# Kernel tuning notes

Hardware: AMD Instinct MI355X
Metric: run time of the kernel (lower is better)

## Reference

```python
import jax, jax.numpy as jnp
import numpy as np

B, S, H, Z = 32, 2048, 256, 64
TEMPERATURE = float(H) ** 0.5
NEG_INF = -1e9


def setup_inputs() -> dict:
    key = jax.random.key(0)
    ks = jax.random.split(key, 8)
    return {
        "encoder_hidden_states": jax.random.normal(ks[0], (B, S, H), dtype=jnp.float32),
        "decoder_hidden_states": jax.random.normal(ks[1], (B, S, H), dtype=jnp.float32),
        "decoder_final_hidden_state": jax.random.normal(ks[2], (B, H), dtype=jnp.float32),
        "latent_z_seq": jax.random.normal(ks[3], (B, S, Z), dtype=jnp.float32),
        "mask": jax.random.randint(ks[4], (B, S), 0, 2).astype(bool),
        "Wq": jax.random.normal(ks[5], (H, H), dtype=jnp.float32),
        "Wk": jax.random.normal(ks[6], (H, H), dtype=jnp.float32),
        "Wv": jax.random.normal(ks[7], (Z, Z), dtype=jnp.float32),
    }


def reference(encoder_hidden_states, decoder_hidden_states, decoder_final_hidden_state,
              latent_z_seq, mask, Wq, Wk, Wv):
    # Projections
    k = jnp.einsum('bsh,hd->bsd', encoder_hidden_states, Wk)
    q = jnp.einsum('bsh,hd->bsd', decoder_hidden_states, Wq)
    v = jnp.einsum('bsz,zd->bsd', latent_z_seq, Wv)
    # alignment[b, i, j] = q_i . k_j / sqrt(H)   -> [B, S, S]
    alignment = jnp.einsum('bid,bjd->bij', q, k) / TEMPERATURE
    # mask over QUERY positions (axis -2), broadcast along key axis (-1)
    alignment = jnp.where(mask[:, :, None], alignment, NEG_INF)
    # NOTE: non-standard softmax over the query axis (dim=-2)
    attn = jax.nn.softmax(alignment, axis=-2)
    output = jnp.einsum('bij,bjd->bid', attn, v)  # [B, S, Z]
    return output, attn
```

## Files before the change

### kernel.cpp

```cpp
#include <hip/hip_runtime.h>
#include <stdint.h>

#define B_  32
#define S_  2048
#define H_  256
#define Z_  64

typedef unsigned short u16;
typedef __attribute__((ext_vector_type(8))) short bf16x8;
typedef __attribute__((ext_vector_type(4))) float f32x4;

__device__ __forceinline__ u16 f2bf(float f) {
    unsigned int x = __float_as_uint(f);
    x = (x + 0x7fffu + ((x >> 16) & 1u)) >> 16;
    return (u16)x;
}
__device__ __forceinline__ float bf2f(u16 u) {
    return __uint_as_float(((unsigned int)u) << 16);
}

__device__ __forceinline__ void gl2lds16(const void* g, void* l) {
    __builtin_amdgcn_global_load_lds(
        (const __attribute__((address_space(1))) unsigned int*)g,
        (__attribute__((address_space(3))) unsigned int*)l,
        16, 0, 0);
}

__global__ void detect_kernel(const u16* __restrict__ wq, int* __restrict__ flag) {
    __shared__ int tot;
    const int t = threadIdx.x;
    if (t == 0) tot = 0;
    __syncthreads();
    int cnt = 0;
    #pragma unroll
    for (int r = 0; r < 16; ++r) {
        u16 u = wq[(r * 256 + t) * 2];
        int e = (u >> 7) & 0xFF;
        cnt += (u == 0 || (e >= 107 && e <= 132)) ? 1 : 0;
    }
    atomicAdd(&tot, cnt);
    __syncthreads();
    if (t == 0) *flag = (tot < 2048) ? 1 : 0;
}

__global__ __launch_bounds__(256) void mask_conv_kernel(const void* __restrict__ raw,
                                                        int* __restrict__ mi) {
    __shared__ int isByte;
    const int t = threadIdx.x;
    if (t == 0) isByte = 0;
    __syncthreads();
    const unsigned int* w = (const unsigned int*)raw;
    if (w[t & 255] > 1u) isByte = 1;
    __syncthreads();
    int e = blockIdx.x * 256 + t;
    int val;
    if (isByte) val = ((const unsigned char*)raw)[e] ? 1 : 0;
    else        val = w[e] ? 1 : 0;
    mi[e] = val;
}

__global__ void wsplit_kernel(const int* __restrict__ flagp,
                              const void* __restrict__ Wq, const void* __restrict__ Wk,
                              u16* __restrict__ WqTh, u16* __restrict__ WqTl,
                              u16* __restrict__ WkTh, u16* __restrict__ WkTl) {
    const int fp32 = *flagp;
    const void* src = blockIdx.y ? Wk : Wq;
    u16* oh = blockIdx.y ? WkTh : WqTh;
    u16* ol = blockIdx.y ? WkTl : WqTl;
    int base = blockIdx.x * 1024;
    #pragma unroll
    for (int r = 0; r < 4; ++r) {
        int idx = base + r * 256 + threadIdx.x;
        int d = idx >> 8, h = idx & 255;
        float v = fp32 ? ((const float*)src)[h * 256 + d]
                       : bf2f(((const u16*)src)[h * 256 + d]);
        u16 hi = f2bf(v);
        oh[idx] = hi;
        ol[idx] = f2bf(v - bf2f(hi));
    }
}

__global__ __launch_bounds__(256) void xsplit_kernel(
        const int* __restrict__ flagp,
        const void* __restrict__ dec, const void* __restrict__ enc,
        u16* __restrict__ Xdh, u16* __restrict__ Xdl,
        u16* __restrict__ Xeh, u16* __restrict__ Xel)
{
    const int fp32 = *flagp;
    const void* src = blockIdx.y ? enc : dec;
    u16* oh = blockIdx.y ? Xeh : Xdh;
    u16* ol = blockIdx.y ? Xel : Xdl;
    const int t = threadIdx.x;
    const size_t blockbase = (size_t)blockIdx.x * 4096;
    if (fp32) {
        const float4* s4 = (const float4*)src;
        #pragma unroll
        for (int j = 0; j < 4; ++j) {
            size_t idx = blockbase + j * 1024 + t * 4;
            float4 v = s4[idx >> 2];
            u16 h0 = f2bf(v.x), h1 = f2bf(v.y), h2 = f2bf(v.z), h3 = f2bf(v.w);
            u16 l0 = f2bf(v.x - bf2f(h0)), l1 = f2bf(v.y - bf2f(h1));
            u16 l2 = f2bf(v.z - bf2f(h2)), l3 = f2bf(v.w - bf2f(h3));
            uint2 ph, pl;
            ph.x = (unsigned)h0 | ((unsigned)h1 << 16);
            ph.y = (unsigned)h2 | ((unsigned)h3 << 16);
            pl.x = (unsigned)l0 | ((unsigned)l1 << 16);
            pl.y = (unsigned)l2 | ((unsigned)l3 << 16);
            ((uint2*)oh)[idx >> 2] = ph;
            ((uint2*)ol)[idx >> 2] = pl;
        }
    } else {
        const uint2* s2 = (const uint2*)src;
        #pragma unroll
        for (int j = 0; j < 4; ++j) {
            size_t idx = blockbase + j * 1024 + t * 4;
            uint2 r = s2[idx >> 2];
            uint2 z; z.x = 0u; z.y = 0u;
            ((uint2*)oh)[idx >> 2] = r;
            ((uint2*)ol)[idx >> 2] = z;
        }
    }
}

__global__ __launch_bounds__(256, 2) void proj_kernel(
        const int* __restrict__ flagp, int use_xsplit,
        const float* __restrict__ Xf, const u16* __restrict__ Xu,
        const u16* __restrict__ Xh, const u16* __restrict__ Xl,
        const u16* __restrict__ WTh, const u16* __restrict__ WTl,
        u16* __restrict__ Ph, u16* __restrict__ Pl)
{
    __shared__ __align__(16) u16 ldsAh[128 * 32];
    __shared__ __align__(16) u16 ldsAl[128 * 32];
    __shared__ __align__(16) u16 ldsBh[128 * 32];
    __shared__ __align__(16) u16 ldsBl[128 * 32];
    const int fp32 = *flagp;
    const int t = threadIdx.x;
    const int lane = t & 63, w = t >> 6;
    const int i0 = blockIdx.x * 128;
    const int d0 = blockIdx.y * 128;
    const int rh = w >> 1, ch = w & 1;
    const int l15 = lane & 15, koff = (lane >> 4) * 8;

    f32x4 acc[4][4];
    #pragma unroll
    for (int a = 0; a < 4; ++a)
        #pragma unroll
        for (int c = 0; c < 4; ++c) acc[a][c] = (f32x4){0.f, 0.f, 0.f, 0.f};

    for (int ks = 0; ks < 8; ++ks) {
        const int kc = ks * 32;
        #pragma unroll
        for (int rep = 0; rep < 2; ++rep) {
            int s = t + rep * 256;
            int r = s >> 2, c8 = (s & 3) * 8;
            gl2lds16(WTh + (size_t)(d0 + r) * H_ + kc + c8, ldsBh + s * 8);
            gl2lds16(WTl + (size_t)(d0 + r) * H_ + kc + c8, ldsBl + s * 8);
            if (use_xsplit) {
                size_t go = (size_t)(i0 + r) * H_ + kc + c8;
                gl2lds16(Xh + go, ldsAh + s * 8);
                gl2lds16(Xl + go, ldsAl + s * 8);
            }
        }
        if (!use_xsplit) {
            if (fp32) {
                #pragma unroll
                for (int rep = 0; rep < 2; ++rep) {
                    int s = t + rep * 256;
                    int r = s >> 2, c8 = (s & 3) * 8;
                    const float4* src = (const float4*)(Xf + (size_t)(i0 + r) * H_ + kc + c8);
                    float4 x0 = src[0], x1 = src[1];
                    float xs[8] = {x0.x, x0.y, x0.z, x0.w, x1.x, x1.y, x1.z, x1.w};
                    unsigned hh[8], ll[8];
                    #pragma unroll
                    for (int j = 0; j < 8; ++j) {
                        u16 hb = f2bf(xs[j]);
                        hh[j] = hb;
                        ll[j] = f2bf(xs[j] - bf2f(hb));
                    }
                    uint4 ph, pl;
                    ph.x = hh[0] | (hh[1] << 16); ph.y = hh[2] | (hh[3] << 16);
                    ph.z = hh[4] | (hh[5] << 16); ph.w = hh[6] | (hh[7] << 16);
                    pl.x = ll[0] | (ll[1] << 16); pl.y = ll[2] | (ll[3] << 16);
                    pl.z = ll[4] | (ll[5] << 16); pl.w = ll[6] | (ll[7] << 16);
                    *(uint4*)(ldsAh + s * 8) = ph;
                    *(uint4*)(ldsAl + s * 8) = pl;
                }
            } else {
                #pragma unroll
                for (int rep = 0; rep < 2; ++rep) {
                    int s = t + rep * 256;
                    int r = s >> 2, c8 = (s & 3) * 8;
                    uint4 raw = *(const uint4*)(Xu + (size_t)(i0 + r) * H_ + kc + c8);
                    *(uint4*)(ldsAh + s * 8) = raw;
                    *(uint4*)(ldsAl + s * 8) = (uint4){0u, 0u, 0u, 0u};
                }
            }
        }
        __syncthreads();
        bf16x8 ah[4], al[4], bh[4], bl[4];
        #pragma unroll
        for (int f = 0; f < 4; ++f) {
            int ar = (rh * 64 + f * 16 + l15) * 32 + koff;
            int br = (ch * 64 + f * 16 + l15) * 32 + koff;
            ah[f] = *(const bf16x8*)(ldsAh + ar);
            al[f] = *(const bf16x8*)(ldsAl + ar);
            bh[f] = *(const bf16x8*)(ldsBh + br);
            bl[f] = *(const bf16x8*)(ldsBl + br);
        }
        #pragma unroll
        for (int fr = 0; fr < 4; ++fr)
            #pragma unroll
            for (int fc = 0; fc < 4; ++fc) {
                acc[fr][fc] = __builtin_amdgcn_mfma_f32_16x16x32_bf16(al[fr], bh[fc], acc[fr][fc], 0, 0, 0);
                acc[fr][fc] = __builtin_amdgcn_mfma_f32_16x16x32_bf16(ah[fr], bl[fc], acc[fr][fc], 0, 0, 0);
                acc[fr][fc] = __builtin_amdgcn_mfma_f32_16x16x32_bf16(ah[fr], bh[fc], acc[fr][fc], 0, 0, 0);
            }
        __syncthreads();
    }
    #pragma unroll
    for (int fr = 0; fr < 4; ++fr)
        #pragma unroll
        for (int fc = 0; fc < 4; ++fc)
            #pragma unroll
            for (int reg = 0; reg < 4; ++reg) {
                float v = acc[fr][fc][reg];
                int i = i0 + rh * 64 + fr * 16 + (lane >> 4) * 4 + reg;
                int d = d0 + ch * 64 + fc * 16 + l15;
                u16 hi = f2bf(v);
                u16 lo = f2bf(v - bf2f(hi));
                size_t off = (size_t)i * H_ + d;
                Ph[off] = hi;
                Pl[off] = lo;
            }
}

__global__ __launch_bounds__(256) void vproj_kernel(
        const int* __restrict__ flagp, const void* __restrict__ Lraw,
        const void* __restrict__ Wvraw, u16* __restrict__ vT)
{
    __shared__ float wv[64 * 16];
    const int fp32 = *flagp;
    const int t = threadIdx.x;
    const int dc = blockIdx.y;
    #pragma unroll
    for (int r = 0; r < 4; ++r) {
        int idx = r * 256 + t;
        int z = idx >> 4, dd = idx & 15;
        wv[idx] = fp32 ? ((const float*)Wvraw)[z * 64 + dc * 16 + dd]
                       : bf2f(((const u16*)Wvraw)[z * 64 + dc * 16 + dd]);
    }
    __syncthreads();
    const int flat = blockIdx.x * 256 + t;
    const int b = flat >> 11, s = flat & 2047;

    float lz[64];
    if (fp32) {
        const float4* lr = (const float4*)((const float*)Lraw + (size_t)flat * 64);
        #pragma unroll
        for (int c = 0; c < 16; ++c) {
            float4 v = lr[c];
            lz[c * 4 + 0] = v.x; lz[c * 4 + 1] = v.y;
            lz[c * 4 + 2] = v.z; lz[c * 4 + 3] = v.w;
        }
    } else {
        const uint4* lr = (const uint4*)((const u16*)Lraw + (size_t)flat * 64);
        #pragma unroll
        for (int c = 0; c < 8; ++c) {
            uint4 v = lr[c];
            unsigned wd[4] = {v.x, v.y, v.z, v.w};
            #pragma unroll
            for (int e2 = 0; e2 < 4; ++e2) {
                lz[c * 8 + e2 * 2 + 0] = bf2f((u16)(wd[e2] & 0xffffu));
                lz[c * 8 + e2 * 2 + 1] = bf2f((u16)(wd[e2] >> 16));
            }
        }
    }

    float acc[16];
    #pragma unroll
    for (int d = 0; d < 16; ++d) acc[d] = 0.f;
    for (int z = 0; z < 64; ++z) {
        float lv = lz[z];
        const float4* wrow = (const float4*)&wv[z * 16];
        #pragma unroll
        for (int d4 = 0; d4 < 4; ++d4) {
            float4 wq = wrow[d4];
            acc[d4 * 4 + 0] += lv * wq.x;
            acc[d4 * 4 + 1] += lv * wq.y;
            acc[d4 * 4 + 2] += lv * wq.z;
            acc[d4 * 4 + 3] += lv * wq.w;
        }
    }
    #pragma unroll
    for (int d = 0; d < 16; ++d)
        vT[((size_t)b * 64 + dc * 16 + d) * S_ + s] = f2bf(acc[d]);
}

__global__ __launch_bounds__(256, 2) void qk_kernel(
        const u16* __restrict__ qh, const u16* __restrict__ ql,
        const u16* __restrict__ kh, const u16* __restrict__ kl,
        const int* __restrict__ maskI, u16* __restrict__ attnB,
        float* __restrict__ attnF, u16* __restrict__ stageB, int use_stage,
        float* __restrict__ m_p, float* __restrict__ s_p,
        int b0, const int* __restrict__ flagp)
{
    __shared__ __align__(16) char smem[35328];
    u16*  stage = (u16*)smem;
    u16*  etile = (u16*)smem;
    float* cmax = (float*)(smem + 32768);
    float* csum = (float*)(smem + 33792);
    float* mrow = (float*)(smem + 34816);

    const int fp32 = *flagp;
    const int t = threadIdx.x;
    const int lane = t & 63, w = t >> 6;
    const int jt = blockIdx.x, it = blockIdx.y, bz = blockIdx.z;
    const int b = b0 + bz;
    const int i0 = it * 128, j0 = jt * 128;
    const int rh = w >> 1, ch = w & 1;
    const int l15 = lane & 15, koff = (lane >> 4) * 8;

    if (t < 128) mrow[t] = (maskI[b * S_ + i0 + t] != 0) ? 1.f : 0.f;

    const size_t qbase = ((size_t)bz * S_ + i0) * H_;
    const size_t kbase = ((size_t)bz * S_ + j0) * H_;

    f32x4 acc[4][4];
    #pragma unroll
    for (int a = 0; a < 4; ++a)
        #pragma unroll
        for (int c = 0; c < 4; ++c) acc[a][c] = (f32x4){0.f, 0.f, 0.f, 0.f};

    for (int ks = 0; ks < 8; ++ks) {
        const int kc = ks * 32;
        #pragma unroll
        for (int rep = 0; rep < 2; ++rep) {
            int s = t + rep * 256;
            int r = s >> 2, c8 = (s & 3) * 8;
            size_t go = (size_t)r * H_ + kc + c8;
            gl2lds16(qh + qbase + go, stage + 0 * 4096 + s * 8);
            gl2lds16(ql + qbase + go, stage + 1 * 4096 + s * 8);
            gl2lds16(kh + kbase + go, stage + 2 * 4096 + s * 8);
            gl2lds16(kl + kbase + go, stage + 3 * 4096 + s * 8);
        }
        __syncthreads();
        bf16x8 ah[4], al[4], bh[4], bl[4];
        #pragma unroll
        for (int f = 0; f < 4; ++f) {
            int ar = (rh * 64 + f * 16 + l15) * 32 + koff;
            int br = (ch * 64 + f * 16 + l15) * 32 + koff;
            ah[f] = *(const bf16x8*)(stage + 0 * 4096 + ar);
            al[f] = *(const bf16x8*)(stage + 1 * 4096 + ar);
            bh[f] = *(const bf16x8*)(stage + 2 * 4096 + br);
            bl[f] = *(const bf16x8*)(stage + 3 * 4096 + br);
        }
        #pragma unroll
        for (int fr = 0; fr < 4; ++fr)
            #pragma unroll
            for (int fc = 0; fc < 4; ++fc) {
                acc[fr][fc] = __builtin_amdgcn_mfma_f32_16x16x32_bf16(al[fr], bh[fc], acc[fr][fc], 0, 0, 0);
                acc[fr][fc] = __builtin_amdgcn_mfma_f32_16x16x32_bf16(ah[fr], bl[fc], acc[fr][fc], 0, 0, 0);
                acc[fr][fc] = __builtin_amdgcn_mfma_f32_16x16x32_bf16(ah[fr], bh[fc], acc[fr][fc], 0, 0, 0);
            }
        __syncthreads();
    }

    const float inv_t = 0.0625f;
    float mloc[4] = {-3e38f, -3e38f, -3e38f, -3e38f};
    #pragma unroll
    for (int fr = 0; fr < 4; ++fr)
        #pragma unroll
        for (int reg = 0; reg < 4; ++reg) {
            float keep = mrow[rh * 64 + fr * 16 + (lane >> 4) * 4 + reg];
            #pragma unroll
            for (int fc = 0; fc < 4; ++fc) {
                float l = acc[fr][fc][reg] * inv_t;
                l = (keep != 0.f) ? l : -1e9f;
                acc[fr][fc][reg] = l;
                mloc[fc] = fmaxf(mloc[fc], l);
            }
        }
    #pragma unroll
    for (int fc = 0; fc < 4; ++fc) {
        mloc[fc] = fmaxf(mloc[fc], __shfl_xor(mloc[fc], 16, 64));
        mloc[fc] = fmaxf(mloc[fc], __shfl_xor(mloc[fc], 32, 64));
    }
    if (lane < 16) {
        #pragma unroll
        for (int fc = 0; fc < 4; ++fc)
            cmax[rh * 128 + ch * 64 + fc * 16 + lane] = mloc[fc];
    }
    __syncthreads();

    float mcol[4], sloc[4];
    #pragma unroll
    for (int fc = 0; fc < 4; ++fc) {
        int c = ch * 64 + fc * 16 + l15;
        mcol[fc] = fmaxf(cmax[c], cmax[128 + c]);
        sloc[fc] = 0.f;
    }
    #pragma unroll
    for (int fr = 0; fr < 4; ++fr)
        #pragma unroll
        for (int reg = 0; reg < 4; ++reg) {
            int row = rh * 64 + fr * 16 + (lane >> 4) * 4 + reg;
            #pragma unroll
            for (int fc = 0; fc < 4; ++fc) {
                float e = __expf(acc[fr][fc][reg] - mcol[fc]);
                sloc[fc] += e;
                etile[row * 128 + ch * 64 + fc * 16 + l15] = f2bf(e);
            }
        }
    #pragma unroll
    for (int fc = 0; fc < 4; ++fc) {
        sloc[fc] += __shfl_xor(sloc[fc], 16, 64);
        sloc[fc] += __shfl_xor(sloc[fc], 32, 64);
    }
    if (lane < 16) {
        #pragma unroll
        for (int fc = 0; fc < 4; ++fc)
            csum[rh * 128 + ch * 64 + fc * 16 + lane] = sloc[fc];
    }
    __syncthreads();

    if (t < 128) {
        float m = fmaxf(cmax[t], cmax[128 + t]);
        float sres = csum[t] + csum[128 + t];
        size_t so = ((size_t)b * 16 + it) * S_ + j0 + t;
        m_p[so] = m;
        s_p[so] = sres;
    }
    const size_t abase = ((size_t)b * S_ + i0) * S_ + j0;
    if (fp32) {
        if (use_stage) {
            #pragma unroll
            for (int rep = 0; rep < 8; ++rep) {
                int s = t + rep * 256;
                int row = s >> 4, off = (s & 15) * 8;
                *(uint4*)(stageB + abase + (size_t)row * S_ + off) = *(const uint4*)(etile + s * 8);
            }
        } else {
            #pragma unroll
            for (int rep = 0; rep < 8; ++rep) {
                int s = t + rep * 256;
                int row = s >> 4, off = (s & 15) * 8;
                const u16* src = etile + s * 8;
                float* gp = attnF + abase + (size_t)row * S_ + off;
                float4 f0, f1;
                f0.x = bf2f(src[0]); f0.y = bf2f(src[1]); f0.z = bf2f(src[2]); f0.w = bf2f(src[3]);
                f1.x = bf2f(src[4]); f1.y = bf2f(src[5]); f1.z = bf2f(src[6]); f1.w = bf2f(src[7]);
                *(float4*)gp = f0;
                *(float4*)(gp + 4) = f1;
            }
        }
    } else {
        #pragma unroll
        for (int rep = 0; rep < 8; ++rep) {
            int s = t + rep * 256;
            int row = s >> 4, off = (s & 15) * 8;
            *(uint4*)(attnB + abase + (size_t)row * S_ + off) = *(const uint4*)(etile + s * 8);
        }
    }
}

__global__ __launch_bounds__(256) void stats_kernel(
        const float* __restrict__ m_p, const float* __restrict__ s_p, float* __restrict__ scl)
{
    int id = blockIdx.x * 256 + threadIdx.x;
    int b = id >> 11, j = id & 2047;
    float mv[16];
    float M = -3e38f;
    #pragma unroll
    for (int itile = 0; itile < 16; ++itile) {
        mv[itile] = m_p[((size_t)b * 16 + itile) * S_ + j];
        M = fmaxf(M, mv[itile]);
    }
    float L = 0.f;
    #pragma unroll
    for (int itile = 0; itile < 16; ++itile)
        L += s_p[((size_t)b * 16 + itile) * S_ + j] * __expf(mv[itile] - M);
    float invL = (L > 0.f) ? (1.f / L) : 0.f;
    #pragma unroll
    for (int itile = 0; itile < 16; ++itile)
        scl[((size_t)b * 16 + itile) * S_ + j] = __expf(mv[itile] - M) * invL;
}

__global__ __launch_bounds__(256, 2) void av_kernel(
        const u16* __restrict__ vT, const float* __restrict__ scl,
        u16* __restrict__ attnB, float* __restrict__ attnF,
        const u16* __restrict__ stageB, int use_stage,
        u16* __restrict__ outB, float* __restrict__ outF,
        const int* __restrict__ flagp)
{
    __shared__ __align__(16) u16 lds_attn[128 * 128];
    __shared__ __align__(16) u16 lds_vt[64 * 128];
    __shared__ float lds_scale[128];
    const int fp32 = *flagp;
    const int t = threadIdx.x;
    const int lane = t & 63, w = t >> 6;
    const int it = blockIdx.x, b = blockIdx.y;
    const int i0 = it * 128;
    const int l15 = lane & 15, koff = (lane >> 4) * 8;

    f32x4 acc[2][4];
    #pragma unroll
    for (int a = 0; a < 2; ++a)
        #pragma unroll
        for (int c = 0; c < 4; ++c) acc[a][c] = (f32x4){0.f, 0.f, 0.f, 0.f};

    for (int jt = 0; jt < 16; ++jt) {
        const int j0 = jt * 128;
        __syncthreads();
        if (t < 128) lds_scale[t] = scl[((size_t)b * 16 + it) * S_ + j0 + t];
        #pragma unroll
        for (int rep = 0; rep < 4; ++rep) {
            int s = t + rep * 256;
            int d = s >> 4, off = (s & 15) * 8;
            gl2lds16(vT + ((size_t)b * 64 + d) * S_ + j0 + off, lds_vt + s * 8);
        }
        __syncthreads();

        const size_t abase = ((size_t)b * S_ + i0) * S_ + j0;
        if (fp32) {
            if (use_stage) {
                #pragma unroll
                for (int rep = 0; rep < 8; ++rep) {
                    int s = t + rep * 256;
                    int row = s >> 4, off = (s & 15) * 8;
                    uint4 pk = *(const uint4*)(stageB + abase + (size_t)row * S_ + off);
                    unsigned wd[4] = {pk.x, pk.y, pk.z, pk.w};
                    float4 f0, f1;
                    f0.x = bf2f((u16)(wd[0] & 0xffffu)) * lds_scale[off + 0];
                    f0.y = bf2f((u16)(wd[0] >> 16))     * lds_scale[off + 1];
                    f0.z = bf2f((u16)(wd[1] & 0xffffu)) * lds_scale[off + 2];
                    f0.w = bf2f((u16)(wd[1] >> 16))     * lds_scale[off + 3];
                    f1.x = bf2f((u16)(wd[2] & 0xffffu)) * lds_scale[off + 4];
                    f1.y = bf2f((u16)(wd[2] >> 16))     * lds_scale[off + 5];
                    f1.z = bf2f((u16)(wd[3] & 0xffffu)) * lds_scale[off + 6];
                    f1.w = bf2f((u16)(wd[3] >> 16))     * lds_scale[off + 7];
                    float* gp = attnF + abase + (size_t)row * S_ + off;
                    *(float4*)gp = f0;
                    *(float4*)(gp + 4) = f1;
                    uint4 opk;
                    opk.x = (unsigned)f2bf(f0.x) | ((unsigned)f2bf(f0.y) << 16);
                    opk.y = (unsigned)f2bf(f0.z) | ((unsigned)f2bf(f0.w) << 16);
                    opk.z = (unsigned)f2bf(f1.x) | ((unsigned)f2bf(f1.y) << 16);
                    opk.w = (unsigned)f2bf(f1.z) | ((unsigned)f2bf(f1.w) << 16);
                    *(uint4*)(lds_attn + s * 8) = opk;
                }
            } else {
                #pragma unroll
                for (int rep = 0; rep < 8; ++rep) {
                    int s = t + rep * 256;
                    int row = s >> 4, off = (s & 15) * 8;
                    float* gp = attnF + abase + (size_t)row * S_ + off;
                    float4 p0 = *(const float4*)gp;
                    float4 p1 = *(const float4*)(gp + 4);
                    p0.x *= lds_scale[off + 0]; p0.y *= lds_scale[off + 1];
                    p0.z *= lds_scale[off + 2]; p0.w *= lds_scale[off + 3];
                    p1.x *= lds_scale[off + 4]; p1.y *= lds_scale[off + 5];
                    p1.z *= lds_scale[off + 6]; p1.w *= lds_scale[off + 7];
                    *(float4*)gp = p0;
                    *(float4*)(gp + 4) = p1;
                    uint4 pk;
                    pk.x = (unsigned)f2bf(p0.x) | ((unsigned)f2bf(p0.y) << 16);
                    pk.y = (unsigned)f2bf(p0.z) | ((unsigned)f2bf(p0.w) << 16);
                    pk.z = (unsigned)f2bf(p1.x) | ((unsigned)f2bf(p1.y) << 16);
                    pk.w = (unsigned)f2bf(p1.z) | ((unsigned)f2bf(p1.w) << 16);
                    *(uint4*)(lds_attn + s * 8) = pk;
                }
            }
        } else {
            #pragma unroll
            for (int rep = 0; rep < 8; ++rep) {
                int s = t + rep * 256;
                int row = s >> 4, off = (s & 15) * 8;
                size_t ga = abase + (size_t)row * S_ + off;
                uint4 pk = *(const uint4*)(attnB + ga);
                unsigned int wd[4] = {pk.x, pk.y, pk.z, pk.w};
                #pragma unroll
                for (int e2 = 0; e2 < 4; ++e2) {
                    float f0 = bf2f((u16)(wd[e2] & 0xffffu)) * lds_scale[off + e2 * 2];
                    float f1 = bf2f((u16)(wd[e2] >> 16))     * lds_scale[off + e2 * 2 + 1];
                    wd[e2] = (unsigned int)f2bf(f0) | ((unsigned int)f2bf(f1) << 16);
                }
                uint4 opk; opk.x = wd[0]; opk.y = wd[1]; opk.z = wd[2]; opk.w = wd[3];
                *(uint4*)(attnB + ga) = opk;
                *(uint4*)(lds_attn + s * 8) = opk;
            }
        }
        __syncthreads();

        #pragma unroll
        for (int ksj = 0; ksj < 4; ++ksj) {
            bf16x8 a0 = *(const bf16x8*)(lds_attn + (w * 32 +  0 + l15) * 128 + ksj * 32 + koff);
            bf16x8 a1 = *(const bf16x8*)(lds_attn + (w * 32 + 16 + l15) * 128 + ksj * 32 + koff);
            bf16x8 bb[4];
            #pragma unroll
            for (int fc = 0; fc < 4; ++fc)
                bb[fc] = *(const bf16x8*)(lds_vt + (fc * 16 + l15) * 128 + ksj * 32 + koff);
            #pragma unroll
            for (int fc = 0; fc < 4; ++fc) {
                acc[0][fc] = __builtin_amdgcn_mfma_f32_16x16x32_bf16(a0, bb[fc], acc[0][fc], 0, 0, 0);
                acc[1][fc] = __builtin_amdgcn_mfma_f32_16x16x32_bf16(a1, bb[fc], acc[1][fc], 0, 0, 0);
            }
        }
    }
    #pragma unroll
    for (int fr = 0; fr < 2; ++fr)
        #pragma unroll
        for (int fc = 0; fc < 4; ++fc)
            #pragma unroll
            for (int reg = 0; reg < 4; ++reg) {
                int i = i0 + w * 32 + fr * 16 + (lane >> 4) * 4 + reg;
                int d = fc * 16 + l15;
                float v = acc[fr][fc][reg];
                size_t oo = ((size_t)b * S_ + i) * Z_ + d;
                if (fp32) outF[oo] = v;
                else      outB[oo] = f2bf(v);
            }
}

extern "C" void kernel_launch(void* const* d_in, const int* in_sizes, int n_in,
                              void* d_out, int out_size, void* d_ws, size_t ws_size,
                              hipStream_t stream) {
    const void* enc    = d_in[0];
    const void* dec    = d_in[1];
    const void* latent = d_in[3];
    const void* mraw   = d_in[4];
    const void* Wq     = d_in[5];
    const void* Wk     = d_in[6];
    const void* Wv     = d_in[7];

    u16*   outB  = (u16*)d_out;
    float* outF  = (float*)d_out;
    u16*   attnB = outB + (size_t)B_ * S_ * Z_;
    float* attnF = outF + (size_t)B_ * S_ * Z_;
    float* m_p = (float*)d_out;
    float* s_p = m_p + (size_t)B_ * 16 * S_;

    char* ws = (char*)d_ws;
    int*   flag  = (int*)ws;
    int*   maskI = (int*)(ws + 256);
    u16*   vT    = (u16*)((char*)maskI + (size_t)B_ * S_ * 4);
    u16*   WqTh  = vT + (size_t)B_ * Z_ * S_;
    u16*   WqTl  = WqTh + H_ * H_;
    u16*   WkTh  = WqTl + H_ * H_;
    u16*   WkTl  = WkTh + H_ * H_;
    float* scl   = (float*)(WkTl + H_ * H_);
    char*  dyn   = (char*)(scl + (size_t)B_ * 16 * S_);

    const size_t fixed_bytes  = (size_t)(dyn - ws);
    const size_t per_batch    = (size_t)4 * S_ * H_ * 2;
    const size_t xsplit_bytes = (size_t)4 * B_ * S_ * H_ * 2;
    const size_t stage_bytes  = (size_t)B_ * S_ * S_ * 2;

    long long avail = (long long)ws_size - (long long)fixed_bytes;
    int use_xsplit = 0, use_stage = 0;
    u16 *Xdh = 0, *Xdl = 0, *Xeh = 0, *Xel = 0, *stageB = 0;
    if (avail >= (long long)(xsplit_bytes + per_batch)) {
        use_xsplit = 1;
        Xdh = (u16*)dyn;
        Xdl = Xdh + (size_t)B_ * S_ * H_;
        Xeh = Xdl + (size_t)B_ * S_ * H_;
        Xel = Xeh + (size_t)B_ * S_ * H_;
        dyn += xsplit_bytes;
        avail -= (long long)xsplit_bytes;
    }
    if (avail >= (long long)(stage_bytes + per_batch)) {
        use_stage = 1;
        stageB = (u16*)dyn;
        dyn += stage_bytes;
        avail -= (long long)stage_bytes;
    }
    int g_b = (avail > 0) ? (int)(avail / (long long)per_batch) : 1;
    if (g_b < 1)  g_b = 1;
    if (g_b > 32) g_b = 32;

    u16* qh = (u16*)dyn;
    u16* ql = qh + (size_t)g_b * S_ * H_;
    u16* kh = ql + (size_t)g_b * S_ * H_;
    u16* kl = kh + (size_t)g_b * S_ * H_;

    detect_kernel<<<dim3(1), 256, 0, stream>>>((const u16*)Wq, flag);
    mask_conv_kernel<<<dim3(256), 256, 0, stream>>>(mraw, maskI);
    wsplit_kernel<<<dim3(64, 2), 256, 0, stream>>>(flag, Wq, Wk, WqTh, WqTl, WkTh, WkTl);
    vproj_kernel<<<dim3(256, 4), 256, 0, stream>>>(flag, latent, Wv, vT);
    if (use_xsplit)
        xsplit_kernel<<<dim3(4096, 2), 256, 0, stream>>>(flag, dec, enc, Xdh, Xdl, Xeh, Xel);

    for (int b0 = 0; b0 < B_; b0 += g_b) {
        int g = (B_ - b0 < g_b) ? (B_ - b0) : g_b;
        size_t eoff = (size_t)b0 * S_ * H_;
        proj_kernel<<<dim3(g * 16, 2), 256, 0, stream>>>(
            flag, use_xsplit, (const float*)dec + eoff, (const u16*)dec + eoff,
            use_xsplit ? Xdh + eoff : (u16*)0, use_xsplit ? Xdl + eoff : (u16*)0,
            WqTh, WqTl, qh, ql);
        proj_kernel<<<dim3(g * 16, 2), 256, 0, stream>>>(
            flag, use_xsplit, (const float*)enc + eoff, (const u16*)enc + eoff,
            use_xsplit ? Xeh + eoff : (u16*)0, use_xsplit ? Xel + eoff : (u16*)0,
            WkTh, WkTl, kh, kl);
        qk_kernel<<<dim3(16, 16, g), 256, 0, stream>>>(qh, ql, kh, kl, maskI,
                                                       attnB, attnF, stageB, use_stage,
                                                       m_p, s_p, b0, flag);
    }
    stats_kernel<<<dim3(256), 256, 0, stream>>>(m_p, s_p, scl);
    av_kernel<<<dim3(16, 32), 256, 0, stream>>>(vT, scl, attnB, attnF, stageB, use_stage,
                                                outB, outF, flag);
}
```

Before: 1.177 ms.

## Swizzle LDS layouts, merge Q/K projections, and split AV into GEMM plus scale pass

```diff
diff --git a/kernel.cpp b/kernel.cpp
--- a/kernel.cpp
+++ b/kernel.cpp
@@ -124,22 +124,40 @@
 
 __global__ __launch_bounds__(256, 2) void proj_kernel(
         const int* __restrict__ flagp, int use_xsplit,
-        const float* __restrict__ Xf, const u16* __restrict__ Xu,
-        const u16* __restrict__ Xh, const u16* __restrict__ Xl,
-        const u16* __restrict__ WTh, const u16* __restrict__ WTl,
-        u16* __restrict__ Ph, u16* __restrict__ Pl)
+        const float* __restrict__ Xf0, const u16* __restrict__ Xu0,
+        const u16* __restrict__ Xh0, const u16* __restrict__ Xl0,
+        const u16* __restrict__ WTh0, const u16* __restrict__ WTl0,
+        u16* __restrict__ Ph0, u16* __restrict__ Pl0,
+        const float* __restrict__ Xf1, const u16* __restrict__ Xu1,
+        const u16* __restrict__ Xh1, const u16* __restrict__ Xl1,
+        const u16* __restrict__ WTh1, const u16* __restrict__ WTl1,
+        u16* __restrict__ Ph1, u16* __restrict__ Pl1)
 {
-    __shared__ __align__(16) u16 ldsAh[128 * 32];
-    __shared__ __align__(16) u16 ldsAl[128 * 32];
-    __shared__ __align__(16) u16 ldsBh[128 * 32];
-    __shared__ __align__(16) u16 ldsBl[128 * 32];
+    __shared__ __align__(16) u16 lds[16384];
+    const int z = blockIdx.z;
+    const float* Xf = z ? Xf1 : Xf0;
+    const u16*   Xu = z ? Xu1 : Xu0;
+    const u16*   Xh = z ? Xh1 : Xh0;
+    const u16*   Xl = z ? Xl1 : Xl0;
+    const u16*  WTh = z ? WTh1 : WTh0;
+    const u16*  WTl = z ? WTl1 : WTl0;
+    u16* Ph = z ? Ph1 : Ph0;
+    u16* Pl = z ? Pl1 : Pl0;
+
     const int fp32 = *flagp;
     const int t = threadIdx.x;
     const int lane = t & 63, w = t >> 6;
     const int i0 = blockIdx.x * 128;
     const int d0 = blockIdx.y * 128;
     const int rh = w >> 1, ch = w & 1;
-    const int l15 = lane & 15, koff = (lane >> 4) * 8;
+    const int l15 = lane & 15;
+    const int c0 = lane >> 4;
+
+    const int srow = t >> 3;
+    const int scp  = t & 7;
+    const int sc   = scp ^ (srow & 7);
+    const int scol = (sc & 3) * 8;
+    const int slo  = sc & 4;
 
     f32x4 acc[4][4];
     #pragma unroll
@@ -149,63 +167,70 @@
 
     for (int ks = 0; ks < 8; ++ks) {
         const int kc = ks * 32;
-        #pragma unroll
-        for (int rep = 0; rep < 2; ++rep) {
-            int s = t + rep * 256;
-            int r = s >> 2, c8 = (s & 3) * 8;
-            gl2lds16(WTh + (size_t)(d0 + r) * H_ + kc + c8, ldsBh + s * 8);
-            gl2lds16(WTl + (size_t)(d0 + r) * H_ + kc + c8, ldsBl + s * 8);
-            if (use_xsplit) {
-                size_t go = (size_t)(i0 + r) * H_ + kc + c8;
-                gl2lds16(Xh + go, ldsAh + s * 8);
-                gl2lds16(Xl + go, ldsAl + s * 8);
-            }
-        }
-        if (!use_xsplit) {
-            if (fp32) {
+        {
+            const u16* wsrc = slo ? WTl : WTh;
+            #pragma unroll
+            for (int rep = 0; rep < 4; ++rep) {
+                int s = t + rep * 256;
+                int row = srow + rep * 32;
+                gl2lds16(wsrc + (size_t)(d0 + row) * H_ + kc + scol, lds + 8192 + s * 8);
+            }
+        }
+        if (use_xsplit) {
+            const u16* xsrc = slo ? Xl : Xh;
+            #pragma unroll
+            for (int rep = 0; rep < 4; ++rep) {
+                int s = t + rep * 256;
+                int row = srow + rep * 32;
+                gl2lds16(xsrc + (size_t)(i0 + row) * H_ + kc + scol, lds + s * 8);
+            }
+        } else if (fp32) {
+            #pragma unroll
+            for (int rep = 0; rep < 2; ++rep) {
+                int s = t + rep * 256;
+                int r = s >> 2, c8 = s & 3;
+                const float4* src = (const float4*)(Xf + (size_t)(i0 + r) * H_ + kc + c8 * 8);
+                float4 x0 = src[0], x1 = src[1];
+                float xs[8] = {x0.x, x0.y, x0.z, x0.w, x1.x, x1.y, x1.z, x1.w};
+                unsigned hh[8], ll[8];
                 #pragma unroll
-                for (int rep = 0; rep < 2; ++rep) {
-                    int s = t + rep * 256;
-                    int r = s >> 2, c8 = (s & 3) * 8;
-                    const float4* src = (const float4*)(Xf + (size_t)(i0 + r) * H_ + kc + c8);
-                    float4 x0 = src[0], x1 = src[1];
-                    float xs[8] = {x0.x, x0.y, x0.z, x0.w, x1.x, x1.y, x1.z, x1.w};
-                    unsigned hh[8], ll[8];
-                    #pragma unroll
-                    for (int j = 0; j < 8; ++j) {
-                        u16 hb = f2bf(xs[j]);
-                        hh[j] = hb;
-                        ll[j] = f2bf(xs[j] - bf2f(hb));
-                    }
-                    uint4 ph, pl;
-                    ph.x = hh[0] | (hh[1] << 16); ph.y = hh[2] | (hh[3] << 16);
-                    ph.z = hh[4] | (hh[5] << 16); ph.w = hh[6] | (hh[7] << 16);
-                    pl.x = ll[0] | (ll[1] << 16); pl.y = ll[2] | (ll[3] << 16);
-                    pl.z = ll[4] | (ll[5] << 16); pl.w = ll[6] | (ll[7] << 16);
-                    *(uint4*)(ldsAh + s * 8) = ph;
-                    *(uint4*)(ldsAl + s * 8) = pl;
+                for (int j = 0; j < 8; ++j) {
+                    u16 hb = f2bf(xs[j]);
+                    hh[j] = hb;
+                    ll[j] = f2bf(xs[j] - bf2f(hb));
                 }
-            } else {
-                #pragma unroll
-                for (int rep = 0; rep < 2; ++rep) {
-                    int s = t + rep * 256;
-                    int r = s >> 2, c8 = (s & 3) * 8;
-                    uint4 raw = *(const uint4*)(Xu + (size_t)(i0 + r) * H_ + kc + c8);
-                    *(uint4*)(ldsAh + s * 8) = raw;
-                    *(uint4*)(ldsAl + s * 8) = (uint4){0u, 0u, 0u, 0u};
-                }
+                uint4 ph, pl;
+                ph.x = hh[0] | (hh[1] << 16); ph.y = hh[2] | (hh[3] << 16);
+                ph.z = hh[4] | (hh[5] << 16); ph.w = hh[6] | (hh[7] << 16);
+                pl.x = ll[0] | (ll[1] << 16); pl.y = ll[2] | (ll[3] << 16);
+                pl.z = ll[4] | (ll[5] << 16); pl.w = ll[6] | (ll[7] << 16);
+                int posH = c8 ^ (r & 7);
+                *(uint4*)(lds + r * 64 + posH * 8) = ph;
+                *(uint4*)(lds + r * 64 + (posH ^ 4) * 8) = pl;
+            }
+        } else {
+            #pragma unroll
+            for (int rep = 0; rep < 2; ++rep) {
+                int s = t + rep * 256;
+                int r = s >> 2, c8 = s & 3;
+                uint4 raw = *(const uint4*)(Xu + (size_t)(i0 + r) * H_ + kc + c8 * 8);
+                int posH = c8 ^ (r & 7);
+                *(uint4*)(lds + r * 64 + posH * 8) = raw;
+                *(uint4*)(lds + r * 64 + (posH ^ 4) * 8) = (uint4){0u, 0u, 0u, 0u};
             }
         }
         __syncthreads();
         bf16x8 ah[4], al[4], bh[4], bl[4];
         #pragma unroll
         for (int f = 0; f < 4; ++f) {
-            int ar = (rh * 64 + f * 16 + l15) * 32 + koff;
-            int br = (ch * 64 + f * 16 + l15) * 32 + koff;
-            ah[f] = *(const bf16x8*)(ldsAh + ar);
-            al[f] = *(const bf16x8*)(ldsAl + ar);
-            bh[f] = *(const bf16x8*)(ldsBh + br);
-            bl[f] = *(const bf16x8*)(ldsBl + br);
+            int ra = rh * 64 + f * 16 + l15;
+            int rb = ch * 64 + f * 16 + l15;
+            int pa = c0 ^ (ra & 7);
+            int pb = c0 ^ (rb & 7);
+            ah[f] = *(const bf16x8*)(lds + ra * 64 + pa * 8);
+            al[f] = *(const bf16x8*)(lds + ra * 64 + (pa ^ 4) * 8);
+            bh[f] = *(const bf16x8*)(lds + 8192 + rb * 64 + pb * 8);
+            bl[f] = *(const bf16x8*)(lds + 8192 + rb * 64 + (pb ^ 4) * 8);
         }
         #pragma unroll
         for (int fr = 0; fr < 4; ++fr)
@@ -318,13 +343,21 @@
     const int b = b0 + bz;
     const int i0 = it * 128, j0 = jt * 128;
     const int rh = w >> 1, ch = w & 1;
-    const int l15 = lane & 15, koff = (lane >> 4) * 8;
+    const int l15 = lane & 15;
+    const int c0 = lane >> 4;
 
     if (t < 128) mrow[t] = (maskI[b * S_ + i0 + t] != 0) ? 1.f : 0.f;
 
     const size_t qbase = ((size_t)bz * S_ + i0) * H_;
     const size_t kbase = ((size_t)bz * S_ + j0) * H_;
 
+    const int srow = t >> 3;
+    const int scp  = t & 7;
+    const int sc   = scp ^ (srow & 7);
+    const int scol = (sc & 3) * 8;
+    const u16* qsrc = (sc & 4) ? ql : qh;
+    const u16* ksrc = (sc & 4) ? kl : kh;
+
     f32x4 acc[4][4];
     #pragma unroll
     for (int a = 0; a < 4; ++a)
@@ -334,25 +367,24 @@
     for (int ks = 0; ks < 8; ++ks) {
         const int kc = ks * 32;
         #pragma unroll
-        for (int rep = 0; rep < 2; ++rep) {
+        for (int rep = 0; rep < 4; ++rep) {
             int s = t + rep * 256;
-            int r = s >> 2, c8 = (s & 3) * 8;
-            size_t go = (size_t)r * H_ + kc + c8;
-            gl2lds16(qh + qbase + go, stage + 0 * 4096 + s * 8);
-            gl2lds16(ql + qbase + go, stage + 1 * 4096 + s * 8);
-            gl2lds16(kh + kbase + go, stage + 2 * 4096 + s * 8);
-            gl2lds16(kl + kbase + go, stage + 3 * 4096 + s * 8);
+            int row = srow + rep * 32;
+            gl2lds16(qsrc + qbase + (size_t)row * H_ + kc + scol, stage + s * 8);
+            gl2lds16(ksrc + kbase + (size_t)row * H_ + kc + scol, stage + 8192 + s * 8);
         }
         __syncthreads();
         bf16x8 ah[4], al[4], bh[4], bl[4];
         #pragma unroll
         for (int f = 0; f < 4; ++f) {
-            int ar = (rh * 64 + f * 16 + l15) * 32 + koff;
-            int br = (ch * 64 + f * 16 + l15) * 32 + koff;
-            ah[f] = *(const bf16x8*)(stage + 0 * 4096 + ar);
-            al[f] = *(const bf16x8*)(stage + 1 * 4096 + ar);
-            bh[f] = *(const bf16x8*)(stage + 2 * 4096 + br);
-            bl[f] = *(const bf16x8*)(stage + 3 * 4096 + br);
+            int ra = rh * 64 + f * 16 + l15;
+            int rb = ch * 64 + f * 16 + l15;
+            int pa = c0 ^ (ra & 7);
+            int pb = c0 ^ (rb & 7);
+            ah[f] = *(const bf16x8*)(stage + ra * 64 + pa * 8);
+            al[f] = *(const bf16x8*)(stage + ra * 64 + (pa ^ 4) * 8);
+            bh[f] = *(const bf16x8*)(stage + 8192 + rb * 64 + pb * 8);
+            bl[f] = *(const bf16x8*)(stage + 8192 + rb * 64 + (pb ^ 4) * 8);
         }
         #pragma unroll
         for (int fr = 0; fr < 4; ++fr)
@@ -485,10 +517,150 @@
         scl[((size_t)b * 16 + itile) * S_ + j] = __expf(mv[itile] - M) * invL;
 }
 
-__global__ __launch_bounds__(256, 2) void av_kernel(
+__global__ __launch_bounds__(256, 2) void av_gemm_kernel(
+        const u16* __restrict__ vT, const float* __restrict__ scl,
+        const u16* __restrict__ stageB, const u16* __restrict__ attnRawB,
+        u16* __restrict__ outB, float* __restrict__ outF,
+        const int* __restrict__ flagp)
+{
+    __shared__ __align__(16) u16 lds_attn[128 * 128];
+    __shared__ __align__(16) u16 lds_vt[64 * 128];
+    const int fp32 = *flagp;
+    const u16* srcE = fp32 ? stageB : attnRawB;
+    const int t = threadIdx.x;
+    const int lane = t & 63, w = t >> 6;
+    const int it = blockIdx.x, b = blockIdx.y;
+    const int i0 = it * 128;
+    const int l15 = lane & 15;
+
+    const int acp = t & 15;
+    const int arow0 = t >> 4;
+    const int ac = acp ^ (arow0 & 15);
+    const int vpos = (t & 15) ^ (t >> 4);
+    const int j8 = (t & 15) * 8;
+
+    f32x4 acc[2][4];
+    #pragma unroll
+    for (int a = 0; a < 2; ++a)
+        #pragma unroll
+        for (int c = 0; c < 4; ++c) acc[a][c] = (f32x4){0.f, 0.f, 0.f, 0.f};
+
+    for (int jt = 0; jt < 16; ++jt) {
+        const int j0 = jt * 128;
+        __syncthreads();
+        const size_t abase = ((size_t)b * S_ + i0) * S_ + j0;
+        #pragma unroll
+        for (int rep = 0; rep < 8; ++rep) {
+            int s = t + rep * 256;
+            int row = arow0 + rep * 16;
+            gl2lds16(srcE + abase + (size_t)row * S_ + ac * 8, lds_attn + s * 8);
+        }
+        float sc[8];
+        {
+            const float4* sp = (const float4*)(scl + ((size_t)b * 16 + it) * S_ + j0 + j8);
+            float4 s0 = sp[0], s1 = sp[1];
+            sc[0] = s0.x; sc[1] = s0.y; sc[2] = s0.z; sc[3] = s0.w;
+            sc[4] = s1.x; sc[5] = s1.y; sc[6] = s1.z; sc[7] = s1.w;
+        }
+        #pragma unroll
+        for (int rep = 0; rep < 4; ++rep) {
+            int d = (t >> 4) + rep * 16;
+            uint4 raw = *(const uint4*)(vT + ((size_t)b * 64 + d) * S_ + j0 + j8);
+            unsigned wd[4] = {raw.x, raw.y, raw.z, raw.w};
+            #pragma unroll
+            for (int e2 = 0; e2 < 4; ++e2) {
+                float f0 = bf2f((u16)(wd[e2] & 0xffffu)) * sc[e2 * 2];
+                float f1 = bf2f((u16)(wd[e2] >> 16))     * sc[e2 * 2 + 1];
+                wd[e2] = (unsigned)f2bf(f0) | ((unsigned)f2bf(f1) << 16);
+            }
+            uint4 pk; pk.x = wd[0]; pk.y = wd[1]; pk.z = wd[2]; pk.w = wd[3];
+            *(uint4*)(lds_vt + d * 128 + vpos * 8) = pk;
+        }
+        __syncthreads();
+
+        #pragma unroll
+        for (int ksj = 0; ksj < 4; ++ksj) {
+            int ck = ksj * 4 + (lane >> 4);
+            int pA = ck ^ l15;
+            int rA0 = w * 32 + l15, rA1 = w * 32 + 16 + l15;
+            bf16x8 a0 = *(const bf16x8*)(lds_attn + rA0 * 128 + pA * 8);
+            bf16x8 a1 = *(const bf16x8*)(lds_attn + rA1 * 128 + pA * 8);
+            bf16x8 bb[4];
+            #pragma unroll
+            for (int fc = 0; fc < 4; ++fc) {
+                int d = fc * 16 + l15;
+                bb[fc] = *(const bf16x8*)(lds_vt + d * 128 + pA * 8);
+            }
+            #pragma unroll
+            for (int fc = 0; fc < 4; ++fc) {
+                acc[0][fc] = __builtin_amdgcn_mfma_f32_16x16x32_bf16(a0, bb[fc], acc[0][fc], 0, 0, 0);
+                acc[1][fc] = __builtin_amdgcn_mfma_f32_16x16x32_bf16(a1, bb[fc], acc[1][fc], 0, 0, 0);
+            }
+        }
+    }
+    #pragma unroll
+    for (int fr = 0; fr < 2; ++fr)
+        #pragma unroll
+        for (int fc = 0; fc < 4; ++fc)
+            #pragma unroll
+            for (int reg = 0; reg < 4; ++reg) {
+                int i = i0 + w * 32 + fr * 16 + (lane >> 4) * 4 + reg;
+                int d = fc * 16 + l15;
+                float v = acc[fr][fc][reg];
+                size_t oo = ((size_t)b * S_ + i) * Z_ + d;
+                if (fp32) outF[oo] = v;
+                else      outB[oo] = f2bf(v);
+            }
+}
+
+__global__ __launch_bounds__(256) void scale_attn_kernel(
+        const u16* stageB, u16* attnB, float* attnF,
+        const float* __restrict__ scl, const int* __restrict__ flagp)
+{
+    const int fp32 = *flagp;
+    const u16* srcE = fp32 ? stageB : attnB;
+    const size_t N8 = (size_t)B_ * S_ * S_ / 8;
+    const size_t stride = (size_t)gridDim.x * 256;
+    for (size_t u = (size_t)blockIdx.x * 256 + threadIdx.x; u < N8; u += stride) {
+        size_t flat = u * 8;
+        int j  = (int)(flat & (S_ - 1));
+        int i  = (int)((flat >> 11) & (S_ - 1));
+        int b  = (int)(flat >> 22);
+        int it = i >> 7;
+        const float* sp = scl + ((size_t)b * 16 + it) * S_ + j;
+        float4 s0 = *(const float4*)sp;
+        float4 s1 = *(const float4*)(sp + 4);
+        uint4 e = *(const uint4*)(srcE + flat);
+        unsigned wd[4] = {e.x, e.y, e.z, e.w};
+        float f[8];
+        f[0] = bf2f((u16)(wd[0] & 0xffffu)) * s0.x;
+        f[1] = bf2f((u16)(wd[0] >> 16))     * s0.y;
+        f[2] = bf2f((u16)(wd[1] & 0xffffu)) * s0.z;
+        f[3] = bf2f((u16)(wd[1] >> 16))     * s0.w;
+        f[4] = bf2f((u16)(wd[2] & 0xffffu)) * s1.x;
+        f[5] = bf2f((u16)(wd[2] >> 16))     * s1.y;
+        f[6] = bf2f((u16)(wd[3] & 0xffffu)) * s1.z;
+        f[7] = bf2f((u16)(wd[3] >> 16))     * s1.w;
+        if (fp32) {
+            float4 o0, o1;
+            o0.x = f[0]; o0.y = f[1]; o0.z = f[2]; o0.w = f[3];
+            o1.x = f[4]; o1.y = f[5]; o1.z = f[6]; o1.w = f[7];
+            *(float4*)(attnF + flat) = o0;
+            *(float4*)(attnF + flat + 4) = o1;
+        } else {
+            uint4 o;
+            o.x = (unsigned)f2bf(f[0]) | ((unsigned)f2bf(f[1]) << 16);
+            o.y = (unsigned)f2bf(f[2]) | ((unsigned)f2bf(f[3]) << 16);
+            o.z = (unsigned)f2bf(f[4]) | ((unsigned)f2bf(f[5]) << 16);
+            o.w = (unsigned)f2bf(f[6]) | ((unsigned)f2bf(f[7]) << 16);
+            *(uint4*)(attnB + flat) = o;
+        }
+    }
+}
+
+__global__ __launch_bounds__(256, 2) void av_fallback_kernel(
         const u16* __restrict__ vT, const float* __restrict__ scl,
         u16* __restrict__ attnB, float* __restrict__ attnF,
-        const u16* __restrict__ stageB, int use_stage,
         u16* __restrict__ outB, float* __restrict__ outF,
         const int* __restrict__ flagp)
 {
@@ -522,53 +694,25 @@
 
         const size_t abase = ((size_t)b * S_ + i0) * S_ + j0;
         if (fp32) {
-            if (use_stage) {
-                #pragma unroll
-                for (int rep = 0; rep < 8; ++rep) {
-                    int s = t + rep * 256;
-                    int row = s >> 4, off = (s & 15) * 8;
-                    uint4 pk = *(const uint4*)(stageB + abase + (size_t)row * S_ + off);
-                    unsigned wd[4] = {pk.x, pk.y, pk.z, pk.w};
-                    float4 f0, f1;
-                    f0.x = bf2f((u16)(wd[0] & 0xffffu)) * lds_scale[off + 0];
-                    f0.y = bf2f((u16)(wd[0] >> 16))     * lds_scale[off + 1];
-                    f0.z = bf2f((u16)(wd[1] & 0xffffu)) * lds_scale[off + 2];
-                    f0.w = bf2f((u16)(wd[1] >> 16))     * lds_scale[off + 3];
-                    f1.x = bf2f((u16)(wd[2] & 0xffffu)) * lds_scale[off + 4];
-                    f1.y = bf2f((u16)(wd[2] >> 16))     * lds_scale[off + 5];
-                    f1.z = bf2f((u16)(wd[3] & 0xffffu)) * lds_scale[off + 6];
-                    f1.w = bf2f((u16)(wd[3] >> 16))     * lds_scale[off + 7];
-                    float* gp = attnF + abase + (size_t)row * S_ + off;
-                    *(float4*)gp = f0;
-                    *(float4*)(gp + 4) = f1;
-                    uint4 opk;
-                    opk.x = (unsigned)f2bf(f0.x) | ((unsigned)f2bf(f0.y) << 16);
-                    opk.y = (unsigned)f2bf(f0.z) | ((unsigned)f2bf(f0.w) << 16);
-                    opk.z = (unsigned)f2bf(f1.x) | ((unsigned)f2bf(f1.y) << 16);
-                    opk.w = (unsigned)f2bf(f1.z) | ((unsigned)f2bf(f1.w) << 16);
-                    *(uint4*)(lds_attn + s * 8) = opk;
-                }
-            } else {
-                #pragma unroll
-                for (int rep = 0; rep < 8; ++rep) {
-                    int s = t + rep * 256;
-                    int row = s >> 4, off = (s & 15) * 8;
-                    float* gp = attnF + abase + (size_t)row * S_ + off;
-                    float4 p0 = *(const float4*)gp;
-                    float4 p1 = *(const float4*)(gp + 4);
-                    p0.x *= lds_scale[off + 0]; p0.y *= lds_scale[off + 1];
-                    p0.z *= lds_scale[off + 2]; p0.w *= lds_scale[off + 3];
-                    p1.x *= lds_scale[off + 4]; p1.y *= lds_scale[off + 5];
-                    p1.z *= lds_scale[off + 6]; p1.w *= lds_scale[off + 7];
-                    *(float4*)gp = p0;
-                    *(float4*)(gp + 4) = p1;
-                    uint4 pk;
-                    pk.x = (unsigned)f2bf(p0.x) | ((unsigned)f2bf(p0.y) << 16);
-                    pk.y = (unsigned)f2bf(p0.z) | ((unsigned)f2bf(p0.w) << 16);
-                    pk.z = (unsigned)f2bf(p1.x) | ((unsigned)f2bf(p1.y) << 16);
-                    pk.w = (unsigned)f2bf(p1.z) | ((unsigned)f2bf(p1.w) << 16);
-                    *(uint4*)(lds_attn + s * 8) = pk;
-                }
+            #pragma unroll
+            for (int rep = 0; rep < 8; ++rep) {
+                int s = t + rep * 256;
+                int row = s >> 4, off = (s & 15) * 8;
+                float* gp = attnF + abase + (size_t)row * S_ + off;
+                float4 p0 = *(const float4*)gp;
+                float4 p1 = *(const float4*)(gp + 4);
+                p0.x *= lds_scale[off + 0]; p0.y *= lds_scale[off + 1];
+                p0.z *= lds_scale[off + 2]; p0.w *= lds_scale[off + 3];
+                p1.x *= lds_scale[off + 4]; p1.y *= lds_scale[off + 5];
+                p1.z *= lds_scale[off + 6]; p1.w *= lds_scale[off + 7];
+                *(float4*)gp = p0;
+                *(float4*)(gp + 4) = p1;
+                uint4 pk;
+                pk.x = (unsigned)f2bf(p0.x) | ((unsigned)f2bf(p0.y) << 16);
+                pk.y = (unsigned)f2bf(p0.z) | ((unsigned)f2bf(p0.w) << 16);
+                pk.z = (unsigned)f2bf(p1.x) | ((unsigned)f2bf(p1.y) << 16);
+                pk.w = (unsigned)f2bf(p1.z) | ((unsigned)f2bf(p1.w) << 16);
+                *(uint4*)(lds_attn + s * 8) = pk;
             }
         } else {
             #pragma unroll
@@ -692,12 +836,12 @@
     for (int b0 = 0; b0 < B_; b0 += g_b) {
         int g = (B_ - b0 < g_b) ? (B_ - b0) : g_b;
         size_t eoff = (size_t)b0 * S_ * H_;
-        proj_kernel<<<dim3(g * 16, 2), 256, 0, stream>>>(
-            flag, use_xsplit, (const float*)dec + eoff, (const u16*)dec + eoff,
+        proj_kernel<<<dim3(g * 16, 2, 2), 256, 0, stream>>>(
+            flag, use_xsplit,
+            (const float*)dec + eoff, (const u16*)dec + eoff,
             use_xsplit ? Xdh + eoff : (u16*)0, use_xsplit ? Xdl + eoff : (u16*)0,
-            WqTh, WqTl, qh, ql);
-        proj_kernel<<<dim3(g * 16, 2), 256, 0, stream>>>(
-            flag, use_xsplit, (const float*)enc + eoff, (const u16*)enc + eoff,
+            WqTh, WqTl, qh, ql,
+            (const float*)enc + eoff, (const u16*)enc + eoff,
             use_xsplit ? Xeh + eoff : (u16*)0, use_xsplit ? Xel + eoff : (u16*)0,
             WkTh, WkTl, kh, kl);
         qk_kernel<<<dim3(16, 16, g), 256, 0, stream>>>(qh, ql, kh, kl, maskI,
@@ -705,6 +849,12 @@
                                                        m_p, s_p, b0, flag);
     }
     stats_kernel<<<dim3(256), 256, 0, stream>>>(m_p, s_p, scl);
-    av_kernel<<<dim3(16, 32), 256, 0, stream>>>(vT, scl, attnB, attnF, stageB, use_stage,
-                                                outB, outF, flag);
-}
+    if (use_stage) {
+        av_gemm_kernel<<<dim3(16, 32), 256, 0, stream>>>(vT, scl, stageB, attnB,
+                                                         outB, outF, flag);
+        scale_attn_kernel<<<dim3(2048), 256, 0, stream>>>(stageB, attnB, attnF, scl, flag);
+    } else {
+        av_fallback_kernel<<<dim3(16, 32), 256, 0, stream>>>(vT, scl, attnB, attnF,
+                                                             outB, outF, flag);
+    }
+}
```

New measurement: 1.211 ms. 1.03x slower.
